# Kernel optimization log

Hardware: AMD Instinct MI355X
Metric: run time of the kernel (lower is better)

The kernel has to match this reference:

```python
import jax, jax.numpy as jnp
import numpy as np

HEADS = 8
LATENT_LEN = 64
SEQ_LEN = 8192
DIM = 512
DIM_HEAD = DIM // HEADS
LN_EPS = 1e-5


def setup_inputs() -> dict:
    key = jax.random.key(0)
    k1, k2, k3 = jax.random.split(key, 3)
    b, n = 16, SEQ_LEN + LATENT_LEN
    x = jax.random.normal(k1, (b, n, DIM), dtype=jnp.float32)
    # torch nn.Linear weights are [out_features, in_features]
    wq = jax.random.normal(k2, (DIM, DIM), dtype=jnp.float32) * (DIM ** -0.5)
    wkv = jax.random.normal(k3, (DIM, DIM), dtype=jnp.float32) * (DIM ** -0.5)
    ln_g = jnp.ones((DIM_HEAD,), dtype=jnp.float32)
    ln_b = jnp.zeros((DIM_HEAD,), dtype=jnp.float32)
    return {"x": x, "wq": wq, "wkv": wkv, "ln_g": ln_g, "ln_b": ln_b}


def _rotate_half(t):
    # lucidrains-style rotate_half: split last dim in two halves, (-x2, x1)
    d2 = t.shape[-1] // 2
    t1, t2 = t[..., :d2], t[..., d2:]
    return jnp.concatenate([-t2, t1], axis=-1)


def _rotary_emb(n, d, dtype):
    inv_freq = 1.0 / (10000.0 ** (jnp.arange(0, d, 2, dtype=jnp.float32) / d))
    freqs = jnp.arange(n, dtype=jnp.float32)[:, None] * inv_freq[None, :]  # [n, d/2]
    emb = jnp.concatenate([freqs, freqs], axis=-1)  # [n, d]
    return jnp.cos(emb).astype(dtype), jnp.sin(emb).astype(dtype)


def reference(x, wq, wkv, ln_g, ln_b):
    b, n, dim = x.shape
    h, d = HEADS, DIM_HEAD
    context_len = n - LATENT_LEN
    scale = d ** -0.5

    q = x @ wq.T   # [b, n, dim]
    kv = x @ wkv.T # [b, n, dim]
    # rearrange 'b n (h d) -> (b h) n d'
    to_bh = lambda t: t.reshape(b, n, h, d).transpose(0, 2, 1, 3).reshape(b * h, n, d)
    q, kv = to_bh(q), to_bh(kv)

    cos, sin = _rotary_emb(n, d, x.dtype)  # [n, d] broadcast over (b h)
    rope = lambda t: t * cos + _rotate_half(t) * sin
    q, kv = rope(q), rope(kv)

    q = q * scale
    q_latent = q[:, context_len:, :]  # [(b h), latent, d]

    # LayerNorm over head dim applied to V (kv)
    mu = jnp.mean(kv, axis=-1, keepdims=True)
    var = jnp.mean(jnp.square(kv - mu), axis=-1, keepdims=True)
    lkv = (kv - mu) * jax.lax.rsqrt(var + LN_EPS) * ln_g + ln_b

    sim = jnp.einsum('bid,bjd->bij', q_latent, kv)  # [(b h), latent, n]
    attn = jax.nn.softmax(sim, axis=-1)
    out = jnp.einsum('bij,bjd->bid', attn, lkv)     # [(b h), latent, d]

    # rearrange '(b h) n d -> b n (h d)'
    out = out.reshape(b, h, LATENT_LEN, d).transpose(0, 2, 1, 3).reshape(b, LATENT_LEN, dim)
    return out
```

## Files before the change

kernel.cpp:

```cpp
#include <hip/hip_runtime.h>
#include <hip/hip_bf16.h>
#include <math.h>

#define SEQ_LEN 8192
#define LAT 64
#define NPOS 8256
#define NBATCH 16
#define NHEADS 8
#define DH 64
#define DIM 512
#define NBH 128
#define NROWS 132096
#define NCHUNK 4
#define NTILES 129

typedef unsigned short u16;
typedef unsigned int   u32;
using short8 = __attribute__((ext_vector_type(8))) short;
using f32x4  = __attribute__((ext_vector_type(4))) float;

static __device__ __forceinline__ float bf2f(u16 u) {
  union { u32 i; float f; } v; v.i = ((u32)u) << 16; return v.f;
}
static __device__ __forceinline__ u16 f2bf(float f) {
  union { float f; u32 i; } v; v.f = f;
  u32 x = v.i;
  return (u16)((x + 0x7fffu + ((x >> 16) & 1u)) >> 16);
}
static __device__ __forceinline__ void gload_lds16(const void* g, void* l) {
  __builtin_amdgcn_global_load_lds(
      (const __attribute__((address_space(1))) unsigned int*)g,
      (__attribute__((address_space(3))) unsigned int*)l, 16, 0, 0);
}

__global__ void k_rtable(float* __restrict__ ctab, float* __restrict__ stab) {
  int idx = blockIdx.x * 256 + threadIdx.x;
  int pos = idx >> 5, i = idx & 31;
  float inv = (float)(1.0 / pow(10000.0, (double)(2 * i) / 64.0));
  float ang = (float)pos * inv;
  ctab[idx] = cosf(ang);
  stab[idx] = sinf(ang);
}

__global__ __launch_bounds__(256) void k_xcast(
    const float* __restrict__ x, const float* __restrict__ wkv,
    u16* __restrict__ xbf, u16* __restrict__ wbf) {
  const size_t NX8 = (size_t)NROWS * DIM / 8;
  const size_t NW8 = (size_t)DIM * DIM / 8;
  size_t total = NX8 + NW8;
  for (size_t i = (size_t)blockIdx.x * 256 + threadIdx.x; i < total;
       i += (size_t)gridDim.x * 256) {
    const float4* src; u32* dst; size_t k;
    if (i < NX8) { src = (const float4*)x;   dst = (u32*)xbf; k = i; }
    else         { src = (const float4*)wkv; dst = (u32*)wbf; k = i - NX8; }
    float4 a = src[2 * k], b = src[2 * k + 1];
    uint4 o;
    o.x = (u32)f2bf(a.x) | ((u32)f2bf(a.y) << 16);
    o.y = (u32)f2bf(a.z) | ((u32)f2bf(a.w) << 16);
    o.z = (u32)f2bf(b.x) | ((u32)f2bf(b.y) << 16);
    o.w = (u32)f2bf(b.z) | ((u32)f2bf(b.w) << 16);
    ((uint4*)dst)[k] = o;
  }
}

__global__ __launch_bounds__(256) void k_qproj(
    const float* __restrict__ x, const float* __restrict__ wq,
    const float* __restrict__ ctab, const float* __restrict__ stab,
    u16* __restrict__ qws) {
  __shared__ __align__(16) float xs[8 * 512];
  int t = threadIdx.x;
  int lr0 = blockIdx.x * 8;
  int batch = lr0 >> 6;
  int lat0 = lr0 & 63;
  for (int u = 0; u < 4; ++u) {
    int e = u * 256 + t;
    int row = e >> 7, c4 = e & 127;
    size_t m = (size_t)batch * NPOS + SEQ_LEN + lat0 + row;
    ((float4*)xs)[e] = ((const float4*)(x + m * DIM))[c4];
  }
  __syncthreads();
  float acc0[8], acc1[8];
#pragma unroll
  for (int r = 0; r < 8; ++r) { acc0[r] = 0.f; acc1[r] = 0.f; }
  const float4* w0 = (const float4*)(wq + (size_t)t * DIM);
  const float4* w1 = (const float4*)(wq + (size_t)(t + 256) * DIM);
  for (int kk = 0; kk < 128; ++kk) {
    float4 a = w0[kk], b = w1[kk];
#pragma unroll
    for (int r = 0; r < 8; ++r) {
      float4 xv = ((const float4*)xs)[r * 128 + kk];
      acc0[r] = fmaf(a.x, xv.x, fmaf(a.y, xv.y, fmaf(a.z, xv.z, fmaf(a.w, xv.w, acc0[r]))));
      acc1[r] = fmaf(b.x, xv.x, fmaf(b.y, xv.y, fmaf(b.z, xv.z, fmaf(b.w, xv.w, acc1[r]))));
    }
  }
  __syncthreads();
#pragma unroll
  for (int r = 0; r < 8; ++r) { xs[r * 512 + t] = acc0[r]; xs[r * 512 + t + 256] = acc1[r]; }
  __syncthreads();
  int rh = t >> 2, sub = t & 3;
  int row = rh >> 3, head = rh & 7;
  int lat = lat0 + row, pos = SEQ_LEN + lat;
  int bh = batch * 8 + head;
  u16* qd = qws + ((size_t)bh * LAT + lat) * DH;
#pragma unroll
  for (int u = 0; u < 8; ++u) {
    int i = sub * 8 + u;
    float v1 = xs[row * 512 + head * 64 + i];
    float v2 = xs[row * 512 + head * 64 + i + 32];
    float cc = ctab[pos * 32 + i], ss = stab[pos * 32 + i];
    qd[i]      = f2bf((v1 * cc - v2 * ss) * 0.125f);
    qd[i + 32] = f2bf((v2 * cc + v1 * ss) * 0.125f);
  }
}

__global__ __launch_bounds__(256) void k_kvgemm(
    const u16* __restrict__ xbf, const u16* __restrict__ wbf,
    const float* __restrict__ ctab, const float* __restrict__ stab,
    u16* __restrict__ kvws, float2* __restrict__ stats) {
  __shared__ __align__(16) char smem[33792];
  u16* As = (u16*)smem;
  u16* Bs = (u16*)(smem + 16384);
  float* Cs = (float*)smem;
  int t = threadIdx.x;
  int lane = t & 63, w = t >> 6;
  int wr = w >> 1, wc = w & 1;
  int c = lane & 15, g = lane >> 4;
  int s = (blockIdx.x & 7) * 516 + (blockIdx.x >> 3);
  int n0 = (s & 3) * 128;
  size_t m0 = (size_t)(s >> 2) * 128;

  f32x4 acc[4][4];
#pragma unroll
  for (int mt = 0; mt < 4; ++mt)
#pragma unroll
    for (int nt = 0; nt < 4; ++nt) acc[mt][nt] = (f32x4){0.f, 0.f, 0.f, 0.f};

  int tr = t >> 3;
  int tcs = ((t & 7) ^ (tr & 7)) << 4;
  const char* agsrc = (const char*)(xbf + (m0 + tr) * DIM) + tcs;
  const char* bgsrc = (const char*)(wbf + (size_t)(n0 + tr) * DIM) + tcs;
  char* aldst = (char*)As + t * 16;
  char* bldst = (char*)Bs + t * 16;

  for (int kt = 0; kt < 8; ++kt) {
    __syncthreads();
    {
      const char* ag = agsrc + kt * 128;
      const char* bg = bgsrc + kt * 128;
#pragma unroll
      for (int u = 0; u < 4; ++u) {
        gload_lds16(ag + (size_t)u * 32 * 1024, aldst + u * 4096);
        gload_lds16(bg + (size_t)u * 32 * 1024, bldst + u * 4096);
      }
    }
    __syncthreads();
#pragma unroll
    for (int ks = 0; ks < 2; ++ks) {
      short8 am[4], bn[4];
#pragma unroll
      for (int mt = 0; mt < 4; ++mt) {
        int row = wr * 64 + mt * 16 + c;
        am[mt] = *(const short8*)((char*)As + row * 128 + ((ks * 64 + g * 16) ^ ((row & 7) << 4)));
      }
#pragma unroll
      for (int nt = 0; nt < 4; ++nt) {
        int row = wc * 64 + nt * 16 + c;
        bn[nt] = *(const short8*)((char*)Bs + row * 128 + ((ks * 64 + g * 16) ^ ((row & 7) << 4)));
      }
#pragma unroll
      for (int mt = 0; mt < 4; ++mt)
#pragma unroll
        for (int nt = 0; nt < 4; ++nt)
          acc[mt][nt] = __builtin_amdgcn_mfma_f32_16x16x32_bf16(am[mt], bn[nt], acc[mt][nt], 0, 0, 0);
    }
  }
  for (int p = 0; p < 2; ++p) {
    __syncthreads();
    if (wr == p) {
#pragma unroll
      for (int mt = 0; mt < 4; ++mt)
#pragma unroll
        for (int nt = 0; nt < 4; ++nt)
#pragma unroll
          for (int r = 0; r < 4; ++r)
            Cs[(mt * 16 + 4 * g + r) * 132 + wc * 64 + nt * 16 + c] = acc[mt][nt][r];
    }
    __syncthreads();
    if (t < 128) {
      int r_ = t & 63, hh = t >> 6;
      float v[64];
      const float4* crow = (const float4*)(Cs + r_ * 132 + hh * 64);
#pragma unroll
      for (int q = 0; q < 16; ++q) {
        float4 f = crow[q];
        v[4 * q] = f.x; v[4 * q + 1] = f.y; v[4 * q + 2] = f.z; v[4 * q + 3] = f.w;
      }
      int mi = (int)(m0 + p * 64 + r_);
      int b = mi / NPOS, pos = mi % NPOS;
      const float* ct = ctab + pos * 32;
      const float* st = stab + pos * 32;
#pragma unroll
      for (int i = 0; i < 32; ++i) {
        float cc = ct[i], ss = st[i];
        float v1 = v[i], v2 = v[i + 32];
        v[i]      = v1 * cc - v2 * ss;
        v[i + 32] = v2 * cc + v1 * ss;
      }
      float sum = 0.f;
#pragma unroll
      for (int e = 0; e < 64; ++e) sum += v[e];
      float mu = sum * 0.015625f;
      float sq = 0.f;
#pragma unroll
      for (int e = 0; e < 64; ++e) { float d = v[e] - mu; sq = fmaf(d, d, sq); }
      float rstd = rsqrtf(sq * 0.015625f + 1e-5f);
      int head = (n0 >> 6) + hh;
      int bh = b * 8 + head;
      u32 pk[32];
#pragma unroll
      for (int e = 0; e < 32; ++e) pk[e] = (u32)f2bf(v[2 * e]) | ((u32)f2bf(v[2 * e + 1]) << 16);
      uint4* dst = (uint4*)(kvws + ((size_t)bh * NPOS + pos) * DH);
#pragma unroll
      for (int u = 0; u < 8; ++u) dst[u] = make_uint4(pk[4 * u], pk[4 * u + 1], pk[4 * u + 2], pk[4 * u + 3]);
      stats[(size_t)bh * NPOS + pos] = make_float2(mu, rstd);
    }
  }
}

__global__ __launch_bounds__(256) void k_attn(
    const u16* __restrict__ qws, const u16* __restrict__ kvws,
    const float2* __restrict__ stats, const float* __restrict__ lng, const float* __restrict__ lnb,
    float* __restrict__ pout, float* __restrict__ pml) {
  __shared__ __align__(16) u16 LT[64 * 64];
  __shared__ __align__(16) u16 Pl[4][16 * 64];
  __shared__ float gl[64], bl[64];
  int t = threadIdx.x;
  int lane = t & 63, w = t >> 6;
  int c = lane & 15, g = lane >> 4;
  int bh = blockIdx.y, chunk = blockIdx.x;
  int tt0 = chunk * 33;
  int tt1 = tt0 + 33; if (tt1 > NTILES) tt1 = NTILES;
  if (t < 64) { gl[t] = lng[t]; bl[t] = lnb[t]; }
  short8 qa[2];
  {
    const u16* qrow = qws + ((size_t)bh * LAT + w * 16 + c) * DH;
    qa[0] = *(const short8*)(qrow + 8 * g);
    qa[1] = *(const short8*)(qrow + 32 + 8 * g);
  }
  f32x4 oacc[4];
#pragma unroll
  for (int nt = 0; nt < 4; ++nt) oacc[nt] = (f32x4){0.f, 0.f, 0.f, 0.f};
  float m_run[4], l_run[4];
#pragma unroll
  for (int r = 0; r < 4; ++r) { m_run[r] = -INFINITY; l_run[r] = 0.f; }
  int sj = t & 63, sw = t >> 6;
  for (int tt = tt0; tt < tt1; ++tt) {
    int j0 = tt * 64;
    __syncthreads();
    {
      const u16* src = kvws + ((size_t)bh * NPOS + j0 + sj) * DH + 16 * sw;
      short8 v0 = *(const short8*)src;
      short8 v1 = *(const short8*)(src + 8);
      float2 stv = stats[(size_t)bh * NPOS + j0 + sj];
      float A = stv.y, C = -stv.x * stv.y;
      char* ltb = (char*)LT;
#pragma unroll
      for (int e = 0; e < 16; ++e) {
        int dd = 16 * sw + e;
        u16 uv = (u16)((e < 8) ? v0[e] : v1[e - 8]);
        float y = fmaf(bf2f(uv), A, C);
        y = fmaf(y, gl[dd], bl[dd]);
        *(u16*)(ltb + dd * 128 + ((2 * sj) ^ ((dd & 7) << 4))) = f2bf(y);
      }
    }
    __syncthreads();
    f32x4 sacc[4];
#pragma unroll
    for (int jn = 0; jn < 4; ++jn) sacc[jn] = (f32x4){0.f, 0.f, 0.f, 0.f};
    const u16* kb = kvws + ((size_t)bh * NPOS + j0) * DH;
#pragma unroll
    for (int ks = 0; ks < 2; ++ks)
#pragma unroll
      for (int jn = 0; jn < 4; ++jn) {
        short8 kf = *(const short8*)(kb + (size_t)(jn * 16 + c) * DH + ks * 32 + 8 * g);
        sacc[jn] = __builtin_amdgcn_mfma_f32_16x16x32_bf16(qa[ks], kf, sacc[jn], 0, 0, 0);
      }
    char* pb = (char*)Pl[w];
#pragma unroll
    for (int r = 0; r < 4; ++r) {
      float mt0 = fmaxf(fmaxf(sacc[0][r], sacc[1][r]), fmaxf(sacc[2][r], sacc[3][r]));
      mt0 = fmaxf(mt0, __shfl_xor(mt0, 1));
      mt0 = fmaxf(mt0, __shfl_xor(mt0, 2));
      mt0 = fmaxf(mt0, __shfl_xor(mt0, 4));
      mt0 = fmaxf(mt0, __shfl_xor(mt0, 8));
      float mnew = fmaxf(m_run[r], mt0);
      float corr = __expf(m_run[r] - mnew);
      m_run[r] = mnew;
      float ts = 0.f;
#pragma unroll
      for (int jn = 0; jn < 4; ++jn) {
        float p = __expf(sacc[jn][r] - mnew);
        sacc[jn][r] = p;
        ts += p;
      }
      ts += __shfl_xor(ts, 1); ts += __shfl_xor(ts, 2);
      ts += __shfl_xor(ts, 4); ts += __shfl_xor(ts, 8);
      l_run[r] = l_run[r] * corr + ts;
#pragma unroll
      for (int nt = 0; nt < 4; ++nt) oacc[nt][r] *= corr;
      int i = 4 * g + r;
      int isw = (i & 7) << 4;
#pragma unroll
      for (int jn = 0; jn < 4; ++jn) {
        int j = jn * 16 + c;
        *(u16*)(pb + i * 128 + ((2 * j) ^ isw)) = f2bf(sacc[jn][r]);
      }
    }
#pragma unroll
    for (int ks = 0; ks < 2; ++ks) {
      short8 pa = *(const short8*)(pb + c * 128 + ((ks * 64 + 16 * g) ^ ((c & 7) << 4)));
#pragma unroll
      for (int nt = 0; nt < 4; ++nt) {
        int dd = nt * 16 + c;
        short8 lv = *(const short8*)((char*)LT + dd * 128 + ((ks * 64 + 16 * g) ^ ((dd & 7) << 4)));
        oacc[nt] = __builtin_amdgcn_mfma_f32_16x16x32_bf16(pa, lv, oacc[nt], 0, 0, 0);
      }
    }
  }
  size_t ob = (size_t)bh * NCHUNK + chunk;
#pragma unroll
  for (int nt = 0; nt < 4; ++nt)
#pragma unroll
    for (int r = 0; r < 4; ++r) {
      int i = w * 16 + 4 * g + r;
      pout[(ob * 64 + i) * 64 + nt * 16 + c] = oacc[nt][r];
    }
  if (c == 0) {
#pragma unroll
    for (int r = 0; r < 4; ++r) {
      int i = w * 16 + 4 * g + r;
      pml[(ob * 2 + 0) * 64 + i] = m_run[r];
      pml[(ob * 2 + 1) * 64 + i] = l_run[r];
    }
  }
}

__global__ __launch_bounds__(256) void k_combine(
    const float* __restrict__ pout, const float* __restrict__ pml, float* __restrict__ out) {
  int bh = blockIdx.x, t = threadIdx.x;
  int i = t >> 2, dq = t & 3;
  float mv[NCHUNK], lv[NCHUNK];
#pragma unroll
  for (int cc = 0; cc < NCHUNK; ++cc) {
    size_t ob = (size_t)bh * NCHUNK + cc;
    mv[cc] = pml[(ob * 2 + 0) * 64 + i];
    lv[cc] = pml[(ob * 2 + 1) * 64 + i];
  }
  float M = fmaxf(fmaxf(mv[0], mv[1]), fmaxf(mv[2], mv[3]));
  float wsum = 0.f, wcf[NCHUNK];
#pragma unroll
  for (int cc = 0; cc < NCHUNK; ++cc) { wcf[cc] = __expf(mv[cc] - M); wsum = fmaf(wcf[cc], lv[cc], wsum); }
  float inv = 1.0f / wsum;
#pragma unroll
  for (int e = 0; e < 16; ++e) {
    int dd = dq * 16 + e;
    float a = 0.f;
#pragma unroll
    for (int cc = 0; cc < NCHUNK; ++cc)
      a = fmaf(wcf[cc], pout[(((size_t)bh * NCHUNK + cc) * 64 + i) * 64 + dd], a);
    out[((size_t)(bh >> 3) * LAT + i) * DIM + (bh & 7) * DH + dd] = a * inv;
  }
}

extern "C" void kernel_launch(void* const* d_in, const int* in_sizes, int n_in,
                              void* d_out, int out_size, void* d_ws, size_t ws_size,
                              hipStream_t stream) {
  const float* x   = (const float*)d_in[0];
  const float* wq  = (const float*)d_in[1];
  const float* wkv = (const float*)d_in[2];
  const float* lng = (const float*)d_in[3];
  const float* lnb = (const float*)d_in[4];
  float* out = (float*)d_out;
  char* ws = (char*)d_ws;
  size_t off = 0;
  auto alloc = [&](size_t bytes) { char* p = ws + off; off += (bytes + 255) & ~(size_t)255; return p; };
  float*  ctab  = (float*)alloc((size_t)NPOS * 32 * 4);
  float*  stab  = (float*)alloc((size_t)NPOS * 32 * 4);
  u16*    qws   = (u16*)alloc((size_t)NBH * LAT * DH * 2);
  u16*    kvws  = (u16*)alloc((size_t)NBH * NPOS * DH * 2);
  float2* stats = (float2*)alloc((size_t)NBH * NPOS * 8);
  float*  pout  = (float*)alloc((size_t)NBH * NCHUNK * 64 * 64 * 4);
  float*  pml   = (float*)alloc((size_t)NBH * NCHUNK * 2 * 64 * 4);
  u16*    xbf   = (u16*)alloc((size_t)NROWS * DIM * 2);
  u16*    wbf   = (u16*)alloc((size_t)DIM * DIM * 2);
  (void)in_sizes; (void)n_in; (void)out_size; (void)ws_size;

  hipLaunchKernelGGL(k_rtable, dim3(NPOS * 32 / 256), dim3(256), 0, stream, ctab, stab);
  hipLaunchKernelGGL(k_xcast, dim3(2048), dim3(256), 0, stream, x, wkv, xbf, wbf);
  hipLaunchKernelGGL(k_qproj, dim3(128), dim3(256), 0, stream, x, wq, ctab, stab, qws);
  hipLaunchKernelGGL(k_kvgemm, dim3(4128), dim3(256), 0, stream, xbf, wbf, ctab, stab, kvws, stats);
  hipLaunchKernelGGL(k_attn, dim3(NCHUNK, NBH), dim3(256), 0, stream, qws, kvws, stats, lng, lnb, pout, pml);
  hipLaunchKernelGGL(k_combine, dim3(NBH), dim3(256), 0, stream, pout, pml, out);
}
```

Baseline: 431.3 us.

## Fuse fp32-to-bf16 cast of x into KV GEMM with double-buffered LDS

Removes the separate pass that casts all of x to bf16 in global memory. The KV GEMM now loads fp32 x directly into registers, converts it, and writes swizzled bf16 tiles to LDS. It also double-buffers the A and B tiles so the next k-tile's loads overlap the current MFMAs. This avoids a full write and re-read of a roughly 135 MB bf16 copy, at the cost of doubling A-tile global read bytes inside the GEMM, a 64KB shared allocation, and higher register use.

```diff
diff --git a/kernel.cpp b/kernel.cpp
--- a/kernel.cpp
+++ b/kernel.cpp
@@ -42,25 +42,16 @@
   stab[idx] = sinf(ang);
 }
 
-__global__ __launch_bounds__(256) void k_xcast(
-    const float* __restrict__ x, const float* __restrict__ wkv,
-    u16* __restrict__ xbf, u16* __restrict__ wbf) {
-  const size_t NX8 = (size_t)NROWS * DIM / 8;
-  const size_t NW8 = (size_t)DIM * DIM / 8;
-  size_t total = NX8 + NW8;
-  for (size_t i = (size_t)blockIdx.x * 256 + threadIdx.x; i < total;
-       i += (size_t)gridDim.x * 256) {
-    const float4* src; u32* dst; size_t k;
-    if (i < NX8) { src = (const float4*)x;   dst = (u32*)xbf; k = i; }
-    else         { src = (const float4*)wkv; dst = (u32*)wbf; k = i - NX8; }
-    float4 a = src[2 * k], b = src[2 * k + 1];
-    uint4 o;
-    o.x = (u32)f2bf(a.x) | ((u32)f2bf(a.y) << 16);
-    o.y = (u32)f2bf(a.z) | ((u32)f2bf(a.w) << 16);
-    o.z = (u32)f2bf(b.x) | ((u32)f2bf(b.y) << 16);
-    o.w = (u32)f2bf(b.z) | ((u32)f2bf(b.w) << 16);
-    ((uint4*)dst)[k] = o;
-  }
+__global__ __launch_bounds__(256) void k_wcast(const float* __restrict__ wkv, u16* __restrict__ wbf) {
+  size_t i = (size_t)blockIdx.x * 256 + threadIdx.x;
+  const float4* src = (const float4*)wkv;
+  float4 a = src[2 * i], b = src[2 * i + 1];
+  uint4 o;
+  o.x = (u32)f2bf(a.x) | ((u32)f2bf(a.y) << 16);
+  o.y = (u32)f2bf(a.z) | ((u32)f2bf(a.w) << 16);
+  o.z = (u32)f2bf(b.x) | ((u32)f2bf(b.y) << 16);
+  o.w = (u32)f2bf(b.z) | ((u32)f2bf(b.w) << 16);
+  ((uint4*)wbf)[i] = o;
 }
 
 __global__ __launch_bounds__(256) void k_qproj(
@@ -113,13 +104,11 @@
   }
 }
 
-__global__ __launch_bounds__(256) void k_kvgemm(
-    const u16* __restrict__ xbf, const u16* __restrict__ wbf,
+__global__ __launch_bounds__(256, 2) void k_kvgemm(
+    const float* __restrict__ x, const u16* __restrict__ wbf,
     const float* __restrict__ ctab, const float* __restrict__ stab,
     u16* __restrict__ kvws, float2* __restrict__ stats) {
-  __shared__ __align__(16) char smem[33792];
-  u16* As = (u16*)smem;
-  u16* Bs = (u16*)(smem + 16384);
+  __shared__ __align__(16) char smem[65536];
   float* Cs = (float*)smem;
   int t = threadIdx.x;
   int lane = t & 63, w = t >> 6;
@@ -135,37 +124,63 @@
 #pragma unroll
     for (int nt = 0; nt < 4; ++nt) acc[mt][nt] = (f32x4){0.f, 0.f, 0.f, 0.f};
 
-  int tr = t >> 3;
-  int tcs = ((t & 7) ^ (tr & 7)) << 4;
-  const char* agsrc = (const char*)(xbf + (m0 + tr) * DIM) + tcs;
-  const char* bgsrc = (const char*)(wbf + (size_t)(n0 + tr) * DIM) + tcs;
-  char* aldst = (char*)As + t * 16;
-  char* bldst = (char*)Bs + t * 16;
-
+  int ar = t >> 3, ac8 = t & 7;
+  const float* axbase = x + (m0 + ar) * DIM + ac8 * 8;
+  int aswz = (ac8 * 16) ^ ((ar & 7) << 4);
+  int tcs = ((t & 7) ^ (ar & 7)) << 4;
+  const char* bgsrc = (const char*)(wbf + (size_t)(n0 + ar) * DIM) + tcs;
+
+  float4 a0[4], a1[4];
+  auto issueA = [&](int kt) {
+#pragma unroll
+    for (int u = 0; u < 4; ++u) {
+      const float* p = axbase + (size_t)u * 32 * DIM + kt * 64;
+      a0[u] = *(const float4*)p;
+      a1[u] = *(const float4*)(p + 4);
+    }
+  };
+  auto issueB = [&](int kt, char* bbuf) {
+    const char* bg = bgsrc + kt * 128;
+    char* bl = bbuf + t * 16;
+#pragma unroll
+    for (int u = 0; u < 4; ++u) gload_lds16(bg + (size_t)u * 32 * 1024, bl + u * 4096);
+  };
+  auto writeA = [&](char* abuf) {
+#pragma unroll
+    for (int u = 0; u < 4; ++u) {
+      short8 o;
+      o[0] = (short)f2bf(a0[u].x); o[1] = (short)f2bf(a0[u].y);
+      o[2] = (short)f2bf(a0[u].z); o[3] = (short)f2bf(a0[u].w);
+      o[4] = (short)f2bf(a1[u].x); o[5] = (short)f2bf(a1[u].y);
+      o[6] = (short)f2bf(a1[u].z); o[7] = (short)f2bf(a1[u].w);
+      *(short8*)(abuf + (u * 32 + ar) * 128 + aswz) = o;
+    }
+  };
+
+  issueA(0);
+  issueB(0, smem + 32768);
+  writeA(smem);
+  __syncthreads();
+
+#pragma unroll
   for (int kt = 0; kt < 8; ++kt) {
-    __syncthreads();
-    {
-      const char* ag = agsrc + kt * 128;
-      const char* bg = bgsrc + kt * 128;
-#pragma unroll
-      for (int u = 0; u < 4; ++u) {
-        gload_lds16(ag + (size_t)u * 32 * 1024, aldst + u * 4096);
-        gload_lds16(bg + (size_t)u * 32 * 1024, bldst + u * 4096);
-      }
-    }
-    __syncthreads();
+    char* Acur = smem + (kt & 1) * 16384;
+    char* Bcur = smem + 32768 + (kt & 1) * 16384;
+    char* Anxt = smem + ((kt & 1) ^ 1) * 16384;
+    char* Bnxt = smem + 32768 + ((kt & 1) ^ 1) * 16384;
+    if (kt < 7) { issueA(kt + 1); issueB(kt + 1, Bnxt); }
 #pragma unroll
     for (int ks = 0; ks < 2; ++ks) {
       short8 am[4], bn[4];
 #pragma unroll
       for (int mt = 0; mt < 4; ++mt) {
         int row = wr * 64 + mt * 16 + c;
-        am[mt] = *(const short8*)((char*)As + row * 128 + ((ks * 64 + g * 16) ^ ((row & 7) << 4)));
+        am[mt] = *(const short8*)(Acur + row * 128 + ((ks * 64 + g * 16) ^ ((row & 7) << 4)));
       }
 #pragma unroll
       for (int nt = 0; nt < 4; ++nt) {
         int row = wc * 64 + nt * 16 + c;
-        bn[nt] = *(const short8*)((char*)Bs + row * 128 + ((ks * 64 + g * 16) ^ ((row & 7) << 4)));
+        bn[nt] = *(const short8*)(Bcur + row * 128 + ((ks * 64 + g * 16) ^ ((row & 7) << 4)));
       }
 #pragma unroll
       for (int mt = 0; mt < 4; ++mt)
@@ -173,7 +188,10 @@
         for (int nt = 0; nt < 4; ++nt)
           acc[mt][nt] = __builtin_amdgcn_mfma_f32_16x16x32_bf16(am[mt], bn[nt], acc[mt][nt], 0, 0, 0);
     }
-  }
+    if (kt < 7) writeA(Anxt);
+    __syncthreads();
+  }
+
   for (int p = 0; p < 2; ++p) {
     __syncthreads();
     if (wr == p) {
@@ -391,14 +409,13 @@
   float2* stats = (float2*)alloc((size_t)NBH * NPOS * 8);
   float*  pout  = (float*)alloc((size_t)NBH * NCHUNK * 64 * 64 * 4);
   float*  pml   = (float*)alloc((size_t)NBH * NCHUNK * 2 * 64 * 4);
-  u16*    xbf   = (u16*)alloc((size_t)NROWS * DIM * 2);
   u16*    wbf   = (u16*)alloc((size_t)DIM * DIM * 2);
   (void)in_sizes; (void)n_in; (void)out_size; (void)ws_size;
 
   hipLaunchKernelGGL(k_rtable, dim3(NPOS * 32 / 256), dim3(256), 0, stream, ctab, stab);
-  hipLaunchKernelGGL(k_xcast, dim3(2048), dim3(256), 0, stream, x, wkv, xbf, wbf);
+  hipLaunchKernelGGL(k_wcast, dim3(DIM * DIM / 8 / 256), dim3(256), 0, stream, wkv, wbf);
   hipLaunchKernelGGL(k_qproj, dim3(128), dim3(256), 0, stream, x, wq, ctab, stab, qws);
-  hipLaunchKernelGGL(k_kvgemm, dim3(4128), dim3(256), 0, stream, xbf, wbf, ctab, stab, kvws, stats);
+  hipLaunchKernelGGL(k_kvgemm, dim3(4128), dim3(256), 0, stream, x, wbf, ctab, stab, kvws, stats);
   hipLaunchKernelGGL(k_attn, dim3(NCHUNK, NBH), dim3(256), 0, stream, qws, kvws, stats, lng, lnb, pout, pml);
   hipLaunchKernelGGL(k_combine, dim3(NBH), dim3(256), 0, stream, pout, pml, out);
 }
```

Measured after the change: 393.5 us. -8.8%, faster.
